# Optimization experiments

Hardware: AMD Instinct MI355X
Metric: run time of the kernel (lower is better)

The kernel has to match this reference:

```python
import jax, jax.numpy as jnp
import numpy as np

N = 30000          # num nodes
E = 480000         # num edges (avg degree 16)
IN = 1024          # in_channels
OUT = 128          # out_channels
MAX_DEG = 48       # static cap on per-node in-degree (incl. self-loop); Poisson(16) max over 30k nodes << 48


def setup_inputs() -> dict:
    key = jax.random.key(0)
    k1, k2, k3 = jax.random.split(key, 3)
    x = jax.random.normal(k1, (N, IN), dtype=jnp.float32)
    edge_index = jax.random.randint(k2, (2, E), 0, N, dtype=jnp.int64)
    W = jax.random.normal(k3, (IN, OUT), dtype=jnp.float32) * (1.0 / np.sqrt(IN))
    b = jnp.zeros((OUT,), dtype=jnp.float32)
    return {"x": x, "edge_index": edge_index, "W": W, "b": b}


def _median_conv(x, edge_index, W, b):
    # linear transform first (as in the torch module)
    h = x @ W                                   # [N, OUT]
    n = x.shape[0]
    # add self-loops
    loop = jnp.arange(n, dtype=edge_index.dtype)
    row = jnp.concatenate([edge_index[0], loop])  # source nodes
    col = jnp.concatenate([edge_index[1], loop])  # destination nodes
    # sort edges by destination (jnp.argsort is stable)
    order = jnp.argsort(col)
    row_s = row[order]
    col_s = col[order]
    x_j = h[row_s]                              # [Etot, OUT] gathered neighbor features
    # per-destination degree and within-segment slot index
    ones = jnp.ones_like(col_s)
    deg = jax.ops.segment_sum(ones, col_s, num_segments=n)      # [N]
    start = jnp.cumsum(deg) - deg                                # segment start offsets
    slot = jnp.arange(col_s.shape[0], dtype=col_s.dtype) - start[col_s]
    # padded dense batch [N, MAX_DEG, OUT]; pads = +inf so they sort to the end
    dense = jnp.full((n, MAX_DEG, h.shape[1]), jnp.inf, dtype=h.dtype)
    dense = dense.at[col_s, slot].set(x_j)
    sdense = jnp.sort(dense, axis=1)
    # torch.median returns the LOWER median: sorted index (deg-1)//2
    med_idx = jnp.maximum(deg - 1, 0) // 2                       # [N]
    out = jnp.take_along_axis(sdense, med_idx[:, None, None], axis=1)[:, 0, :]
    # zero-degree nodes would yield +inf; self-loops guarantee deg>=1, but guard anyway
    out = jnp.where((deg > 0)[:, None], out, jnp.zeros_like(out))
    return out + b


def reference(x, edge_index, W, b):
    return _median_conv(x, edge_index, W, b)
```

## Files before the change

### kernel.cpp

```cpp
#include <hip/hip_runtime.h>
#include <hip/hip_bf16.h>

#define N_NODES 30000
#define N_EDGES 480000
#define IN_CH   1024
#define OUT_CH  128
#define MAX_DEG 48

typedef float   f32x4  __attribute__((ext_vector_type(4)));
typedef __bf16  bf16x8 __attribute__((ext_vector_type(8)));
typedef unsigned short ushort8 __attribute__((ext_vector_type(8)));

__device__ __forceinline__ unsigned short f2bf(float f) {
  unsigned int u = __builtin_bit_cast(unsigned int, f);
  u += 0x7fffu + ((u >> 16) & 1u);
  return (unsigned short)(u >> 16);
}

__global__ __launch_bounds__(256) void convert_W(const float* __restrict__ W,
                                                 unsigned short* __restrict__ Wt) {
  int idx = blockIdx.x * 256 + threadIdx.x;
  int n = idx >> 10;
  int k = idx & 1023;
  Wt[idx] = f2bf(W[k * OUT_CH + n]);
}

__global__ __launch_bounds__(256) void build_adj(const int* __restrict__ ei,
                                                 int* __restrict__ deg,
                                                 int* __restrict__ adj) {
  int i = blockIdx.x * blockDim.x + threadIdx.x;
  const int total = N_EDGES + N_NODES;
  if (i >= total) return;
  int src, dst;
  if (i < N_EDGES) { src = ei[i]; dst = ei[N_EDGES + i]; }
  else             { src = i - N_EDGES; dst = src; }
  int slot = atomicAdd(&deg[dst], 1);
  if (slot < MAX_DEG) adj[dst * MAX_DEG + slot] = src;
}

__global__ __launch_bounds__(256) void gemm_h(const float* __restrict__ x,
                                              const unsigned short* __restrict__ Wt,
                                              float* __restrict__ h) {
  const int tid  = threadIdx.x;
  const int wave = tid >> 6;
  const int lane = tid & 63;
  const int l16  = lane & 15;
  const int g4   = lane >> 4;
  const int m0   = blockIdx.x * 64;
  const int arow = m0 + wave * 16 + l16;
  const float* aptr = x + (size_t)(arow < N_NODES ? arow : 0) * IN_CH + g4 * 8;
  const unsigned short* bptr = Wt + l16 * IN_CH + g4 * 8;

  f32x4 acc[8];
#pragma unroll
  for (int i = 0; i < 8; ++i) acc[i] = (f32x4){0.f, 0.f, 0.f, 0.f};

  for (int k0 = 0; k0 < IN_CH; k0 += 32) {
    f32x4 a0 = *(const f32x4*)(aptr + k0);
    f32x4 a1 = *(const f32x4*)(aptr + k0 + 4);
    ushort8 af;
    af[0] = f2bf(a0[0]); af[1] = f2bf(a0[1]); af[2] = f2bf(a0[2]); af[3] = f2bf(a0[3]);
    af[4] = f2bf(a1[0]); af[5] = f2bf(a1[1]); af[6] = f2bf(a1[2]); af[7] = f2bf(a1[3]);
    bf16x8 av = __builtin_bit_cast(bf16x8, af);
#pragma unroll
    for (int nn = 0; nn < 8; ++nn) {
      ushort8 bu = *(const ushort8*)(bptr + nn * 16 * IN_CH + k0);
      bf16x8 bv = __builtin_bit_cast(bf16x8, bu);
      acc[nn] = __builtin_amdgcn_mfma_f32_16x16x32_bf16(av, bv, acc[nn], 0, 0, 0);
    }
  }

  const int crow = m0 + wave * 16 + g4 * 4;
#pragma unroll
  for (int nn = 0; nn < 8; ++nn) {
#pragma unroll
    for (int i = 0; i < 4; ++i) {
      int r = crow + i;
      if (r < N_NODES) h[(size_t)r * OUT_CH + nn * 16 + l16] = acc[nn][i];
    }
  }
}

template <int NS>
__device__ __forceinline__ void batcher_sort(float (&a)[NS]) {
#pragma unroll
  for (int p = 1; p < NS; p <<= 1) {
#pragma unroll
    for (int k = p; k >= 1; k >>= 1) {
#pragma unroll
      for (int j = k % p; j + k < NS; j += 2 * k) {
#pragma unroll
        for (int i = 0; i < k; ++i) {
          if (i + j + k < NS) {
            if ((i + j) / (2 * p) == (i + j + k) / (2 * p)) {
              float lo = fminf(a[i + j], a[i + j + k]);
              float hi = fmaxf(a[i + j], a[i + j + k]);
              a[i + j] = lo;
              a[i + j + k] = hi;
            }
          }
        }
      }
    }
  }
}

template <int NS>
__device__ __forceinline__ float med_n(const float* __restrict__ h,
                                       const int* nbrs, int d, int m, int ch) {
  float a[NS];
#pragma unroll
  for (int j = 0; j < NS; ++j) {
    if (j < d) a[j] = h[(size_t)nbrs[j] * OUT_CH + ch];
    else       a[j] = 1e30f;
  }
  batcher_sort<NS>(a);
  float med = a[0];
#pragma unroll
  for (int j = 1; j < NS; ++j) med = (j == m) ? a[j] : med;
  return med;
}

__global__ __launch_bounds__(128) void median_kernel(const float* __restrict__ h,
                                                     const int* __restrict__ adj,
                                                     const int* __restrict__ deg,
                                                     const float* __restrict__ b,
                                                     float* __restrict__ out) {
  __shared__ int nbrs[64];
  const int node = blockIdx.x;
  const int ch   = threadIdx.x;
  int d = deg[node];
  if (d > MAX_DEG) d = MAX_DEG;
  if (ch < 64) nbrs[ch] = (ch < d && ch < MAX_DEG) ? adj[node * MAX_DEG + ch] : 0;
  __syncthreads();
  const int m = (d - 1) >> 1;

  float med;
  if (d <= 8)       med = med_n<8>(h, nbrs, d, m, ch);
  else if (d <= 16) med = med_n<16>(h, nbrs, d, m, ch);
  else if (d <= 32) med = med_n<32>(h, nbrs, d, m, ch);
  else              med = med_n<64>(h, nbrs, d, m, ch);

  out[(size_t)node * OUT_CH + ch] = med + b[ch];
}

extern "C" void kernel_launch(void* const* d_in, const int* in_sizes, int n_in,
                              void* d_out, int out_size, void* d_ws, size_t ws_size,
                              hipStream_t stream) {
  const float* x  = (const float*)d_in[0];
  const int*   ei = (const int*)d_in[1];
  const float* W  = (const float*)d_in[2];
  const float* b  = (const float*)d_in[3];
  float* out = (float*)d_out;

  char* ws = (char*)d_ws;
  float*          h   = (float*)ws;
  unsigned short* Wt  = (unsigned short*)(ws + 15360000);
  int*            deg = (int*)(ws + 15360000 + 262144);
  int*            adj = (int*)(ws + 15360000 + 262144 + 120000);

  hipMemsetAsync(deg, 0, N_NODES * sizeof(int), stream);
  convert_W<<<dim3(131072 / 256), dim3(256), 0, stream>>>(W, Wt);
  build_adj<<<dim3((N_EDGES + N_NODES + 255) / 256), dim3(256), 0, stream>>>(ei, deg, adj);
  gemm_h<<<dim3((N_NODES + 63) / 64), dim3(256), 0, stream>>>(x, Wt, h);
  median_kernel<<<dim3(N_NODES), dim3(128), 0, stream>>>(h, adj, deg, b, out);
}
```

Before: 314.0 us.

## Split GEMM K-dimension across waves with LDS reduction and fold bias into h

The GEMM now gives each block 16 rows instead of 64, and its four waves each cover a quarter of the K dimension. Partial accumulators are reduced through padded shared memory by wave 0. This launches four times as many blocks, giving more parallelism and a fully unrolled, shorter K loop per wave, at the cost of an LDS round trip and a barrier. The bias is added in the GEMM instead of the median kernel; this is valid because median(v+b) equals median(v)+b.

```diff
diff --git a/kernel.cpp b/kernel.cpp
--- a/kernel.cpp
+++ b/kernel.cpp
@@ -38,24 +38,29 @@
   if (slot < MAX_DEG) adj[dst * MAX_DEG + slot] = src;
 }
 
+#define RED_STRIDE 36
+
 __global__ __launch_bounds__(256) void gemm_h(const float* __restrict__ x,
                                               const unsigned short* __restrict__ Wt,
+                                              const float* __restrict__ b,
                                               float* __restrict__ h) {
   const int tid  = threadIdx.x;
   const int wave = tid >> 6;
   const int lane = tid & 63;
   const int l16  = lane & 15;
   const int g4   = lane >> 4;
-  const int m0   = blockIdx.x * 64;
-  const int arow = m0 + wave * 16 + l16;
-  const float* aptr = x + (size_t)(arow < N_NODES ? arow : 0) * IN_CH + g4 * 8;
-  const unsigned short* bptr = Wt + l16 * IN_CH + g4 * 8;
+  const int m0   = blockIdx.x * 16;
+  const int arow = m0 + l16;
+  const int kbase = wave * 256 + g4 * 8;
+  const float* aptr = x + (size_t)arow * IN_CH + kbase;
+  const unsigned short* bptr = Wt + l16 * IN_CH + kbase;
 
   f32x4 acc[8];
 #pragma unroll
   for (int i = 0; i < 8; ++i) acc[i] = (f32x4){0.f, 0.f, 0.f, 0.f};
 
-  for (int k0 = 0; k0 < IN_CH; k0 += 32) {
+#pragma unroll
+  for (int k0 = 0; k0 < 256; k0 += 32) {
     f32x4 a0 = *(const f32x4*)(aptr + k0);
     f32x4 a1 = *(const f32x4*)(aptr + k0 + 4);
     ushort8 af;
@@ -70,13 +75,34 @@
     }
   }
 
-  const int crow = m0 + wave * 16 + g4 * 4;
+  __shared__ float red[3 * 64 * RED_STRIDE];
+  if (wave >= 1) {
+    float* dst = &red[((wave - 1) * 64 + lane) * RED_STRIDE];
 #pragma unroll
-  for (int nn = 0; nn < 8; ++nn) {
+    for (int nn = 0; nn < 8; ++nn)
+      *(f32x4*)(dst + nn * 4) = acc[nn];
+  }
+  __syncthreads();
+  if (wave == 0) {
 #pragma unroll
-    for (int i = 0; i < 4; ++i) {
-      int r = crow + i;
-      if (r < N_NODES) h[(size_t)r * OUT_CH + nn * 16 + l16] = acc[nn][i];
+    for (int s = 0; s < 3; ++s) {
+      const float* src = &red[(s * 64 + lane) * RED_STRIDE];
+#pragma unroll
+      for (int nn = 0; nn < 8; ++nn) {
+        f32x4 v = *(const f32x4*)(src + nn * 4);
+        acc[nn] += v;
+      }
+    }
+    const int crow = m0 + g4 * 4;
+#pragma unroll
+    for (int nn = 0; nn < 8; ++nn) {
+      const int col = nn * 16 + l16;
+      const float bias = b[col];
+#pragma unroll
+      for (int i = 0; i < 4; ++i) {
+        int r = crow + i;
+        h[(size_t)r * OUT_CH + col] = acc[nn][i] + bias;
+      }
     }
   }
 }
@@ -124,7 +150,6 @@
 __global__ __launch_bounds__(128) void median_kernel(const float* __restrict__ h,
                                                      const int* __restrict__ adj,
                                                      const int* __restrict__ deg,
-                                                     const float* __restrict__ b,
                                                      float* __restrict__ out) {
   __shared__ int nbrs[64];
   const int node = blockIdx.x;
@@ -141,7 +166,7 @@
   else if (d <= 32) med = med_n<32>(h, nbrs, d, m, ch);
   else              med = med_n<64>(h, nbrs, d, m, ch);
 
-  out[(size_t)node * OUT_CH + ch] = med + b[ch];
+  out[(size_t)node * OUT_CH + ch] = med;
 }
 
 extern "C" void kernel_launch(void* const* d_in, const int* in_sizes, int n_in,
@@ -162,6 +187,6 @@
   hipMemsetAsync(deg, 0, N_NODES * sizeof(int), stream);
   convert_W<<<dim3(131072 / 256), dim3(256), 0, stream>>>(W, Wt);
   build_adj<<<dim3((N_EDGES + N_NODES + 255) / 256), dim3(256), 0, stream>>>(ei, deg, adj);
-  gemm_h<<<dim3((N_NODES + 63) / 64), dim3(256), 0, stream>>>(x, Wt, h);
-  median_kernel<<<dim3(N_NODES), dim3(128), 0, stream>>>(h, adj, deg, b, out);
+  gemm_h<<<dim3(N_NODES / 16), dim3(256), 0, stream>>>(x, Wt, b, h);
+  median_kernel<<<dim3(N_NODES), dim3(128), 0, stream>>>(h, adj, deg, out);
 }
```

Measured after the change: 323.0 us. 2.8% more time.

## Restructure GEMM with double-buffered LDS staging via global_load_lds and fold bias

Applied to the files above, without the earlier changes.

Rewrites the x@W GEMM to stage 128x64 fp32 tiles of x into LDS with direct global-to-LDS loads, double-buffered so the next tile loads while the current one is computed. Each wave now covers 128 rows by 32 columns, with an XOR swizzle to avoid LDS bank conflicts. This raises reuse of the W fragments and hides x load latency in what is a memory-bound 120MB read. The bias add moves into the GEMM epilogue, which is exact because the median commutes with adding a per-channel constant. Larger tiles mean fewer blocks (235) than CUs times occupancy, which could reduce parallelism.

```diff
diff --git a/kernel.cpp b/kernel.cpp
--- a/kernel.cpp
+++ b/kernel.cpp
@@ -7,6 +7,10 @@
 #define OUT_CH  128
 #define MAX_DEG 48
 
+#define BM 128
+#define BK 64
+#define NSTEP (IN_CH / BK)
+
 typedef float   f32x4  __attribute__((ext_vector_type(4)));
 typedef __bf16  bf16x8 __attribute__((ext_vector_type(8)));
 typedef unsigned short ushort8 __attribute__((ext_vector_type(8)));
@@ -15,6 +19,12 @@
   unsigned int u = __builtin_bit_cast(unsigned int, f);
   u += 0x7fffu + ((u >> 16) & 1u);
   return (unsigned short)(u >> 16);
+}
+
+__device__ __forceinline__ void gload_lds16(const float* g, float* l) {
+  __builtin_amdgcn_global_load_lds(
+      (const __attribute__((address_space(1))) void*)g,
+      (__attribute__((address_space(3))) void*)l, 16, 0, 0);
 }
 
 __global__ __launch_bounds__(256) void convert_W(const float* __restrict__ W,
@@ -40,43 +50,90 @@
 
 __global__ __launch_bounds__(256) void gemm_h(const float* __restrict__ x,
                                               const unsigned short* __restrict__ Wt,
+                                              const float* __restrict__ bias,
                                               float* __restrict__ h) {
+  __shared__ float smem[2 * BM * BK];
   const int tid  = threadIdx.x;
   const int wave = tid >> 6;
   const int lane = tid & 63;
   const int l16  = lane & 15;
   const int g4   = lane >> 4;
-  const int m0   = blockIdx.x * 64;
-  const int arow = m0 + wave * 16 + l16;
-  const float* aptr = x + (size_t)(arow < N_NODES ? arow : 0) * IN_CH + g4 * 8;
-  const unsigned short* bptr = Wt + l16 * IN_CH + g4 * 8;
-
-  f32x4 acc[8];
-#pragma unroll
-  for (int i = 0; i < 8; ++i) acc[i] = (f32x4){0.f, 0.f, 0.f, 0.f};
-
-  for (int k0 = 0; k0 < IN_CH; k0 += 32) {
-    f32x4 a0 = *(const f32x4*)(aptr + k0);
-    f32x4 a1 = *(const f32x4*)(aptr + k0 + 4);
-    ushort8 af;
-    af[0] = f2bf(a0[0]); af[1] = f2bf(a0[1]); af[2] = f2bf(a0[2]); af[3] = f2bf(a0[3]);
-    af[4] = f2bf(a1[0]); af[5] = f2bf(a1[1]); af[6] = f2bf(a1[2]); af[7] = f2bf(a1[3]);
-    bf16x8 av = __builtin_bit_cast(bf16x8, af);
-#pragma unroll
-    for (int nn = 0; nn < 8; ++nn) {
-      ushort8 bu = *(const ushort8*)(bptr + nn * 16 * IN_CH + k0);
-      bf16x8 bv = __builtin_bit_cast(bf16x8, bu);
-      acc[nn] = __builtin_amdgcn_mfma_f32_16x16x32_bf16(av, bv, acc[nn], 0, 0, 0);
-    }
-  }
-
-  const int crow = m0 + wave * 16 + g4 * 4;
-#pragma unroll
-  for (int nn = 0; nn < 8; ++nn) {
-#pragma unroll
-    for (int i = 0; i < 4; ++i) {
-      int r = crow + i;
-      if (r < N_NODES) h[(size_t)r * OUT_CH + nn * 16 + l16] = acc[nn][i];
+  const int m0   = blockIdx.x * BM;
+  const int trow = tid >> 4;
+  const int tcol = tid & 15;
+
+  f32x4 acc[8][2];
+#pragma unroll
+  for (int rf = 0; rf < 8; ++rf)
+#pragma unroll
+    for (int cf = 0; cf < 2; ++cf) acc[rf][cf] = (f32x4){0.f, 0.f, 0.f, 0.f};
+
+  auto stage = [&](int buf, int st) {
+    const int k0 = st * BK;
+#pragma unroll
+    for (int r = 0; r < 8; ++r) {
+      int row_t = r * 16 + trow;
+      int row_g = m0 + row_t;
+      if (row_g > N_NODES - 1) row_g = N_NODES - 1;
+      int ksw = (tcol ^ (row_t & 7)) << 2;
+      const float* src = x + (size_t)row_g * IN_CH + k0 + ksw;
+      float* dst = smem + buf * (BM * BK) + row_t * BK + tcol * 4;
+      gload_lds16(src, dst);
+    }
+  };
+
+  auto compute = [&](int buf, int st) {
+    const int k0 = st * BK;
+    const char* sb = (const char*)(smem + buf * (BM * BK));
+#pragma unroll
+    for (int ks = 0; ks < 2; ++ks) {
+      bf16x8 bfr[2];
+#pragma unroll
+      for (int cf = 0; cf < 2; ++cf) {
+        int col = wave * 32 + cf * 16 + l16;
+        ushort8 bu = *(const ushort8*)(Wt + (size_t)col * IN_CH + k0 + ks * 32 + g4 * 8);
+        bfr[cf] = __builtin_bit_cast(bf16x8, bu);
+      }
+#pragma unroll
+      for (int rf = 0; rf < 8; ++rf) {
+        int row = rf * 16 + l16;
+        int s   = (row & 7) << 4;
+        int b0  = (row << 8) + ((ks * 32 + g4 * 8) << 2);
+        f32x4 a0 = *(const f32x4*)(sb + ((b0) ^ s));
+        f32x4 a1 = *(const f32x4*)(sb + ((b0 + 16) ^ s));
+        ushort8 af;
+        af[0] = f2bf(a0[0]); af[1] = f2bf(a0[1]); af[2] = f2bf(a0[2]); af[3] = f2bf(a0[3]);
+        af[4] = f2bf(a1[0]); af[5] = f2bf(a1[1]); af[6] = f2bf(a1[2]); af[7] = f2bf(a1[3]);
+        bf16x8 av = __builtin_bit_cast(bf16x8, af);
+        acc[rf][0] = __builtin_amdgcn_mfma_f32_16x16x32_bf16(av, bfr[0], acc[rf][0], 0, 0, 0);
+        acc[rf][1] = __builtin_amdgcn_mfma_f32_16x16x32_bf16(av, bfr[1], acc[rf][1], 0, 0, 0);
+      }
+    }
+  };
+
+  stage(0, 0);
+  __syncthreads();
+  int cur = 0;
+  for (int st = 0; st < NSTEP - 1; ++st) {
+    stage(cur ^ 1, st + 1);
+    compute(cur, st);
+    __syncthreads();
+    cur ^= 1;
+  }
+  compute(cur, NSTEP - 1);
+
+  const int crow0 = m0 + g4 * 4;
+#pragma unroll
+  for (int cf = 0; cf < 2; ++cf) {
+    const int col = wave * 32 + cf * 16 + l16;
+    const float bv = bias[col];
+#pragma unroll
+    for (int rf = 0; rf < 8; ++rf) {
+#pragma unroll
+      for (int i = 0; i < 4; ++i) {
+        int r = crow0 + rf * 16 + i;
+        if (r < N_NODES) h[(size_t)r * OUT_CH + col] = acc[rf][cf][i] + bv;
+      }
     }
   }
 }
@@ -124,7 +181,6 @@
 __global__ __launch_bounds__(128) void median_kernel(const float* __restrict__ h,
                                                      const int* __restrict__ adj,
                                                      const int* __restrict__ deg,
-                                                     const float* __restrict__ b,
                                                      float* __restrict__ out) {
   __shared__ int nbrs[64];
   const int node = blockIdx.x;
@@ -141,7 +197,7 @@
   else if (d <= 32) med = med_n<32>(h, nbrs, d, m, ch);
   else              med = med_n<64>(h, nbrs, d, m, ch);
 
-  out[(size_t)node * OUT_CH + ch] = med + b[ch];
+  out[(size_t)node * OUT_CH + ch] = med;
 }
 
 extern "C" void kernel_launch(void* const* d_in, const int* in_sizes, int n_in,
@@ -162,6 +218,6 @@
   hipMemsetAsync(deg, 0, N_NODES * sizeof(int), stream);
   convert_W<<<dim3(131072 / 256), dim3(256), 0, stream>>>(W, Wt);
   build_adj<<<dim3((N_EDGES + N_NODES + 255) / 256), dim3(256), 0, stream>>>(ei, deg, adj);
-  gemm_h<<<dim3((N_NODES + 63) / 64), dim3(256), 0, stream>>>(x, Wt, h);
-  median_kernel<<<dim3(N_NODES), dim3(128), 0, stream>>>(h, adj, deg, b, out);
-}
+  gemm_h<<<dim3((N_NODES + BM - 1) / BM), dim3(256), 0, stream>>>(x, Wt, b, h);
+  median_kernel<<<dim3(N_NODES), dim3(128), 0, stream>>>(h, adj, deg, out);
+}
```

After: 294.8 us. 6.1% less time.
